# Kernel tuning notes

Hardware: AMD Instinct MI355X
Metric: run time of the kernel (lower is better)

The kernel has to match this reference:

```python
import jax, jax.numpy as jnp
import numpy as np
import math

B, S, H = 2, 2048, 4096
NH, HD = 32, 128            # num_heads, head_dim
Q_RANK, KV_RANK = 1536, 512 # low-rank dims
VD = 128                    # v_head_dim


def setup_inputs() -> dict:
    key = jax.random.key(0)
    ks = jax.random.split(key, 7)
    s = 0.02
    return {
        "hidden_states": jax.random.normal(ks[0], (B, S, H), dtype=jnp.float32),
        "w_qa":  jax.random.normal(ks[1], (H, Q_RANK), dtype=jnp.float32) * s,
        "w_qb":  jax.random.normal(ks[2], (Q_RANK, NH * HD), dtype=jnp.float32) * s,
        "w_kva": jax.random.normal(ks[3], (H, KV_RANK), dtype=jnp.float32) * s,
        "w_kb":  jax.random.normal(ks[4], (KV_RANK, NH * HD), dtype=jnp.float32) * s,
        "w_vb":  jax.random.normal(ks[5], (KV_RANK, NH * VD), dtype=jnp.float32) * s,
        "w_o":   jax.random.normal(ks[6], (NH * VD, H), dtype=jnp.float32) * s,
    }


def reference(hidden_states, w_qa, w_qb, w_kva, w_kb, w_vb, w_o):
    b, s, _ = hidden_states.shape
    # low-rank Q path
    q_c = hidden_states @ w_qa                       # [B,S,q_rank]
    q = (q_c @ w_qb).reshape(b, s, NH, HD)           # [B,S,NH,HD]
    # low-rank compressed KV (this is the cache tensor)
    compressed_kv = hidden_states @ w_kva            # [B,S,kv_rank]
    k = (compressed_kv @ w_kb).reshape(b, s, NH, HD)
    v = (compressed_kv @ w_vb).reshape(b, s, NH, VD)
    # causal SDPA, scale 1/sqrt(head_dim) (position_ids=None -> RoPE no-op)
    scale = 1.0 / math.sqrt(HD)
    scores = jnp.einsum('bqhd,bkhd->bhqk', q, k) * scale
    causal = jnp.tril(jnp.ones((s, s), dtype=bool))
    scores = jnp.where(causal, scores, jnp.finfo(scores.dtype).min)
    attn = jax.nn.softmax(scores, axis=-1)
    out = jnp.einsum('bhqk,bkhd->bqhd', attn, v).reshape(b, s, NH * VD)
    attn_output = out @ w_o                          # [B,S,H]
    return (attn_output, compressed_kv)
```

## Files before the change

### kernel.cpp

```cpp
#include <hip/hip_runtime.h>
#include <hip/hip_bf16.h>
#include <math.h>

#define BB 2
#define SS 2048
#define HH 4096
#define NHEADS 32
#define HDIM 128
#define VDIM 128
#define QRANK 1536
#define KVRANK 512
#define MROWS (BB * SS)

typedef unsigned short u16;
typedef unsigned int u32;
typedef short short8 __attribute__((ext_vector_type(8)));
typedef float floatx4 __attribute__((ext_vector_type(4)));

#if __has_builtin(__builtin_amdgcn_exp2f)
__device__ __forceinline__ float fast_exp2(float x) { return __builtin_amdgcn_exp2f(x); }
#else
__device__ __forceinline__ float fast_exp2(float x) { return exp2f(x); }
#endif

__device__ __forceinline__ u16 f2bf(float f) {
    u32 u = __float_as_uint(f);
    u += 0x7fffu + ((u >> 16) & 1u);
    return (u16)(u >> 16);
}

#define GLD16(gp, lp)                                                        \
    __builtin_amdgcn_global_load_lds(                                        \
        (const __attribute__((address_space(1))) void*)(gp),                 \
        (__attribute__((address_space(3))) void*)(lp), 16, 0, 0)

__global__ __launch_bounds__(256) void cvt_bf16(const float* __restrict__ in,
                                                u16* __restrict__ out, int n4) {
    int idx = blockIdx.x * 256 + threadIdx.x;
    int stride = gridDim.x * 256;
    for (int i = idx; i < n4; i += stride) {
        float4 f = ((const float4*)in)[i];
        u32 lo = (u32)f2bf(f.x) | ((u32)f2bf(f.y) << 16);
        u32 hi = (u32)f2bf(f.z) | ((u32)f2bf(f.w) << 16);
        ((uint2*)out)[i] = make_uint2(lo, hi);
    }
}

__global__ __launch_bounds__(256) void transpose_cvt(const float* __restrict__ in,
                                                     u16* __restrict__ out,
                                                     int R, int C) {
    __shared__ u16 T[64][65];
    const int c0 = blockIdx.x * 64, r0 = blockIdx.y * 64;
    const int tx = threadIdx.x & 63, ty = threadIdx.x >> 6;
#pragma unroll
    for (int p = 0; p < 16; ++p) {
        int rr = p * 4 + ty;
        T[rr][tx] = f2bf(in[(size_t)(r0 + rr) * C + c0 + tx]);
    }
    __syncthreads();
#pragma unroll
    for (int p = 0; p < 16; ++p) {
        int cc = p * 4 + ty;
        out[(size_t)(c0 + cc) * R + r0 + tx] = T[tx][cc];
    }
}

__global__ __launch_bounds__(256) void transpose_v(const u16* __restrict__ in, int ldin,
                                                   u16* __restrict__ out) {
    __shared__ u16 T[64][65];
    const int s0 = blockIdx.x * 64, d0 = blockIdx.y * 64;
    const int bh = blockIdx.z, b = bh >> 5, h = bh & 31;
    const int tx = threadIdx.x & 63, ty = threadIdx.x >> 6;
#pragma unroll
    for (int p = 0; p < 16; ++p) {
        int ss = p * 4 + ty;
        T[ss][tx] = in[(size_t)(b * SS + s0 + ss) * ldin + h * 128 + d0 + tx];
    }
    __syncthreads();
#pragma unroll
    for (int p = 0; p < 16; ++p) {
        int dd = p * 4 + ty;
        out[((size_t)bh * 128 + d0 + dd) * SS + s0 + tx] = T[tx][dd];
    }
}

template <int MODE>
__global__ __launch_bounds__(256) void gemm_bt(const u16* __restrict__ A, int lda,
                                               const u16* __restrict__ Bt, int ldb,
                                               float* __restrict__ Cf, int ldf,
                                               u16* __restrict__ Cb, int ldc,
                                               int M, int N, int K, int nsplit) {
    __shared__ __align__(16) u16 As[128 * 32];
    __shared__ __align__(16) u16 Bs[128 * 32];

    const int tid = threadIdx.x;
    const int bm0 = blockIdx.y * 128, bn0 = blockIdx.x * 128;
    const int w = tid >> 6, lane = tid & 63;
    const int lo = lane & 15, quad = lane >> 4;
    const int wm = (w & 1) * 64, wn = (w >> 1) * 64;

    floatx4 acc[4][4];
#pragma unroll
    for (int i = 0; i < 4; ++i)
#pragma unroll
        for (int j = 0; j < 4; ++j) acc[i][j] = (floatx4){0.f, 0.f, 0.f, 0.f};

    const int o0 = tid * 16, o1 = tid * 16 + 4096;
    const int ar0 = o0 >> 6, ak0 = (o0 & 63) >> 1;
    const int ar1 = o1 >> 6, ak1 = (o1 & 63) >> 1;
    const u16* Ab = A + (size_t)bm0 * lda;
    const u16* Bb = Bt + (size_t)bn0 * ldb;

    for (int k0 = 0; k0 < K; k0 += 32) {
        GLD16(Ab + (size_t)ar0 * lda + k0 + ak0, &As[o0 >> 1]);
        GLD16(Ab + (size_t)ar1 * lda + k0 + ak1, &As[o1 >> 1]);
        GLD16(Bb + (size_t)ar0 * ldb + k0 + ak0, &Bs[o0 >> 1]);
        GLD16(Bb + (size_t)ar1 * ldb + k0 + ak1, &Bs[o1 >> 1]);
        asm volatile("s_waitcnt vmcnt(0)" ::: "memory");
        __syncthreads();

        short8 af[4], bfr[4];
#pragma unroll
        for (int i = 0; i < 4; ++i)
            af[i] = *(const short8*)&As[(wm + i * 16 + lo) * 32 + quad * 8];
#pragma unroll
        for (int j = 0; j < 4; ++j)
            bfr[j] = *(const short8*)&Bs[(wn + j * 16 + lo) * 32 + quad * 8];
#pragma unroll
        for (int i = 0; i < 4; ++i)
#pragma unroll
            for (int j = 0; j < 4; ++j)
                acc[i][j] = __builtin_amdgcn_mfma_f32_16x16x32_bf16(af[i], bfr[j], acc[i][j], 0, 0, 0);
        __syncthreads();
    }

#pragma unroll
    for (int i = 0; i < 4; ++i) {
#pragma unroll
        for (int j = 0; j < 4; ++j) {
            const int row = bm0 + wm + i * 16 + quad * 4;
            const int col = bn0 + wn + j * 16 + lo;
#pragma unroll
            for (int r = 0; r < 4; ++r) {
                float v = acc[i][j][r];
                if (MODE == 0) Cf[(size_t)(row + r) * ldf + col] = v;
                if (MODE == 1) Cb[(size_t)(row + r) * ldc + col] = f2bf(v);
                if (MODE == 3) {
                    Cb[(size_t)(row + r) * ldc + col] = f2bf(v);
                    if (col >= nsplit) Cf[(size_t)(row + r) * ldf + (col - nsplit)] = v;
                }
            }
        }
    }
}

__global__ __launch_bounds__(256) void mla_attn_mfma(const u16* __restrict__ qm,
                                                     const u16* __restrict__ km, int ldk,
                                                     const u16* __restrict__ vt,
                                                     u16* __restrict__ ao) {
    __shared__ __align__(16) u16 Ks[64 * 128];
    __shared__ __align__(16) u16 Vt[(128 + 16) * 64];
    __shared__ __align__(16) u16 Ps[128 * 68];

    const int qt = 15 - blockIdx.y;
    const int bh = blockIdx.x;
    const int b = bh >> 5, h = bh & 31;
    const int tid = threadIdx.x;
    const int w = tid >> 6, lane = tid & 63;
    const int lo = lane & 15, quad = lane >> 4;
    const int q0 = qt * 128;

    const float SCALE_L2E = 0.08838834764831845f * 1.4426950408889634f;

    {
        u32* p = (u32*)&Vt[128 * 64];
        for (int i = tid; i < 512; i += 256) p[i] = 0x3F803F80u;
    }

    const u16* kbase = km + (size_t)(b * SS) * ldk + h * 128;
    const u16* vtbase = vt + (size_t)bh * 128 * SS;
    const int nkt = 2 * qt + 2;

    int ol_[4], kgo[4], vgo[4];
#pragma unroll
    for (int p = 0; p < 4; ++p) {
        int o = tid * 16 + p * 4096;
        int key = o >> 8, ch = (o & 255) >> 4;
        kgo[p] = key * ldk + ((ch ^ (key & 15)) << 3);
        int d = o >> 7, ch2 = (o & 127) >> 4;
        vgo[p] = d * SS + ((ch2 ^ (d & 7)) << 3);
        ol_[p] = o >> 1;
    }

#pragma unroll
    for (int p = 0; p < 4; ++p) GLD16(kbase + kgo[p], &Ks[ol_[p]]);
#pragma unroll
    for (int p = 0; p < 4; ++p) GLD16(vtbase + vgo[p], &Vt[ol_[p]]);

    short8 qf[2][4];
#pragma unroll
    for (int mf = 0; mf < 2; ++mf) {
        const u16* qrow = qm + (size_t)(b * SS + q0 + w * 32 + mf * 16 + lo) * HH + h * 128;
#pragma unroll
        for (int ks = 0; ks < 4; ++ks) qf[mf][ks] = *(const short8*)(qrow + ks * 32 + quad * 8);
    }

    floatx4 oacc[2][8], olv[2];
#pragma unroll
    for (int mf = 0; mf < 2; ++mf) {
        olv[mf] = (floatx4){0.f, 0.f, 0.f, 0.f};
#pragma unroll
        for (int n = 0; n < 8; ++n) oacc[mf][n] = (floatx4){0.f, 0.f, 0.f, 0.f};
    }

    __syncthreads();

    for (int kt = 0; kt < nkt; ++kt) {
        const bool need_mask = (kt >= nkt - 2);
        const bool notlast = (kt + 1 < nkt);

#pragma unroll
        for (int mf = 0; mf < 2; ++mf) {
            floatx4 s[4];
#pragma unroll
            for (int nf = 0; nf < 4; ++nf) s[nf] = (floatx4){0.f, 0.f, 0.f, 0.f};
            __builtin_amdgcn_s_setprio(1);
#pragma unroll
            for (int nf = 0; nf < 4; ++nf)
#pragma unroll
                for (int ks = 0; ks < 4; ++ks) {
                    short8 kf = *(const short8*)&Ks[(nf * 16 + lo) * 128 + (((ks * 4 + quad) ^ lo) << 3)];
                    s[nf] = __builtin_amdgcn_mfma_f32_16x16x32_bf16(qf[mf][ks], kf, s[nf], 0, 0, 0);
                }
            __builtin_amdgcn_s_setprio(0);
#pragma unroll
            for (int nf = 0; nf < 4; ++nf)
#pragma unroll
                for (int r = 0; r < 4; ++r) {
                    float p = fast_exp2(s[nf][r] * SCALE_L2E);
                    if (need_mask) {
                        int kgi = kt * 64 + nf * 16 + lo;
                        int qg = q0 + w * 32 + mf * 16 + quad * 4 + r;
                        p = (kgi <= qg) ? p : 0.f;
                    }
                    Ps[(w * 32 + mf * 16 + quad * 4 + r) * 68 + nf * 16 + lo] = f2bf(p);
                }
        }

        __syncthreads();

        if (notlast) {
            const u16* kn = kbase + (size_t)(kt + 1) * 64 * ldk;
#pragma unroll
            for (int p = 0; p < 4; ++p) GLD16(kn + kgo[p], &Ks[ol_[p]]);
        }

#pragma unroll
        for (int mf = 0; mf < 2; ++mf) {
            short8 pa[2];
#pragma unroll
            for (int ks2 = 0; ks2 < 2; ++ks2)
                pa[ks2] = *(const short8*)&Ps[(w * 32 + mf * 16 + lo) * 68 + ks2 * 32 + quad * 8];
            __builtin_amdgcn_s_setprio(1);
#pragma unroll
            for (int n = 0; n < 8; ++n)
#pragma unroll
                for (int ks2 = 0; ks2 < 2; ++ks2) {
                    short8 vf = *(const short8*)&Vt[(n * 16 + lo) * 64 + (((ks2 * 4 + quad) ^ (lo & 7)) << 3)];
                    oacc[mf][n] = __builtin_amdgcn_mfma_f32_16x16x32_bf16(pa[ks2], vf, oacc[mf][n], 0, 0, 0);
                }
#pragma unroll
            for (int ks2 = 0; ks2 < 2; ++ks2) {
                short8 vf = *(const short8*)&Vt[(128 + lo) * 64 + (((ks2 * 4 + quad) ^ (lo & 7)) << 3)];
                olv[mf] = __builtin_amdgcn_mfma_f32_16x16x32_bf16(pa[ks2], vf, olv[mf], 0, 0, 0);
            }
            __builtin_amdgcn_s_setprio(0);
        }

        __syncthreads();

        if (notlast) {
            const u16* vn = vtbase + (size_t)(kt + 1) * 64;
#pragma unroll
            for (int p = 0; p < 4; ++p) GLD16(vn + vgo[p], &Vt[ol_[p]]);
        }
    }

#pragma unroll
    for (int mf = 0; mf < 2; ++mf) {
        u16* obase = ao + (size_t)(b * SS + q0 + w * 32 + mf * 16 + quad * 4) * HH + h * 128;
#pragma unroll
        for (int r = 0; r < 4; ++r) {
            float inv = 1.f / olv[mf][r];
#pragma unroll
            for (int n = 0; n < 8; ++n)
                obase[(size_t)r * HH + n * 16 + lo] = f2bf(oacc[mf][n][r] * inv);
        }
    }
}

extern "C" void kernel_launch(void* const* d_in, const int* in_sizes, int n_in,
                              void* d_out, int out_size, void* d_ws, size_t ws_size,
                              hipStream_t stream) {
    const float* hs    = (const float*)d_in[0];
    const float* w_qa  = (const float*)d_in[1];
    const float* w_qb  = (const float*)d_in[2];
    const float* w_kva = (const float*)d_in[3];
    const float* w_kb  = (const float*)d_in[4];
    const float* w_vb  = (const float*)d_in[5];
    const float* w_o   = (const float*)d_in[6];

    float* out   = (float*)d_out;
    float* ckv_f = out + (size_t)MROWS * HH;

    u16* ws = (u16*)d_ws;
    u16* hs_bf    = ws;
    u16* vt       = ws;
    u16* q_bf     = ws + 16777216ull;
    u16* kv_bf    = ws + 33554432ull;
    u16* ao_bf    = ws + 67108864ull;
    u16* wqa_kvaT = ws + 83886080ull;
    u16* w_qbT    = ws + 92274688ull;
    u16* wkv_bT   = ws + 98566144ull;
    u16* w_oT     = ws + 102760448ull;
    u16* qc_ckv   = ws + 119537664ull;

    dim3 blk(256);

    cvt_bf16<<<2048, blk, 0, stream>>>(hs, hs_bf, (MROWS * HH) / 4);
    transpose_cvt<<<dim3(QRANK / 64, HH / 64), blk, 0, stream>>>(w_qa, wqa_kvaT, HH, QRANK);
    transpose_cvt<<<dim3(KVRANK / 64, HH / 64), blk, 0, stream>>>(w_kva, wqa_kvaT + 1536ull * 4096, HH, KVRANK);
    transpose_cvt<<<dim3(HH / 64, QRANK / 64), blk, 0, stream>>>(w_qb, w_qbT, QRANK, HH);
    transpose_cvt<<<dim3(HH / 64, KVRANK / 64), blk, 0, stream>>>(w_kb, wkv_bT, KVRANK, HH);
    transpose_cvt<<<dim3(HH / 64, KVRANK / 64), blk, 0, stream>>>(w_vb, wkv_bT + 4096ull * 512, KVRANK, HH);
    transpose_cvt<<<dim3(HH / 64, HH / 64), blk, 0, stream>>>(w_o, w_oT, HH, HH);

    gemm_bt<3><<<dim3(2048 / 128, MROWS / 128), blk, 0, stream>>>(
        hs_bf, HH, wqa_kvaT, HH, ckv_f, KVRANK, qc_ckv, 2048, MROWS, 2048, HH, QRANK);
    gemm_bt<1><<<dim3(HH / 128, MROWS / 128), blk, 0, stream>>>(
        qc_ckv, 2048, w_qbT, QRANK, nullptr, 0, q_bf, HH, MROWS, HH, QRANK, 0);
    gemm_bt<1><<<dim3(8192 / 128, MROWS / 128), blk, 0, stream>>>(
        qc_ckv + 1536, 2048, wkv_bT, KVRANK, nullptr, 0, kv_bf, 8192, MROWS, 8192, KVRANK, 0);
    transpose_v<<<dim3(SS / 64, VDIM / 64, BB * NHEADS), blk, 0, stream>>>(kv_bf + 4096, 8192, vt);
    mla_attn_mfma<<<dim3(BB * NHEADS, 16), blk, 0, stream>>>(q_bf, kv_bf, 8192, vt, ao_bf);
    gemm_bt<0><<<dim3(HH / 128, MROWS / 128), blk, 0, stream>>>(
        ao_bf, HH, w_oT, HH, out, HH, nullptr, 0, MROWS, HH, HH, 0);
}
```

Measured before the change: 811.2 us.

## Use 256x256 GEMM tiles with 4-stage async LDS pipeline and swizzle

Rewrites the bf16 GEMM to use 256x256 output tiles with 512 threads (8 waves, 128x64 per wave). Global-to-LDS loads now go through a 4-deep ring buffer with counted vmcnt waits, so loads overlap with MFMA work instead of waiting for all loads each k-step. An XOR swizzle on the LDS column chunk reduces bank conflicts, and s_setprio raises wave priority during the MFMA bursts. The trade-off is more LDS (128KB) and more registers per block, which lowers occupancy, and fewer blocks per GEMM (e.g. 128 for the first GEMM), which can leave CUs underused.

```diff
diff --git a/kernel.cpp b/kernel.cpp
--- a/kernel.cpp
+++ b/kernel.cpp
@@ -85,64 +85,97 @@
 }
 
 template <int MODE>
-__global__ __launch_bounds__(256) void gemm_bt(const u16* __restrict__ A, int lda,
+__global__ __launch_bounds__(512) void gemm_bt(const u16* __restrict__ A, int lda,
                                                const u16* __restrict__ Bt, int ldb,
                                                float* __restrict__ Cf, int ldf,
                                                u16* __restrict__ Cb, int ldc,
                                                int M, int N, int K, int nsplit) {
-    __shared__ __align__(16) u16 As[128 * 32];
-    __shared__ __align__(16) u16 Bs[128 * 32];
+    __shared__ __align__(16) u16 As[4][256 * 32];
+    __shared__ __align__(16) u16 Bs[4][256 * 32];
 
     const int tid = threadIdx.x;
-    const int bm0 = blockIdx.y * 128, bn0 = blockIdx.x * 128;
+    const int bm0 = blockIdx.y * 256, bn0 = blockIdx.x * 256;
     const int w = tid >> 6, lane = tid & 63;
     const int lo = lane & 15, quad = lane >> 4;
-    const int wm = (w & 1) * 64, wn = (w >> 1) * 64;
-
-    floatx4 acc[4][4];
-#pragma unroll
-    for (int i = 0; i < 4; ++i)
-#pragma unroll
-        for (int j = 0; j < 4; ++j) acc[i][j] = (floatx4){0.f, 0.f, 0.f, 0.f};
-
-    const int o0 = tid * 16, o1 = tid * 16 + 4096;
-    const int ar0 = o0 >> 6, ak0 = (o0 & 63) >> 1;
-    const int ar1 = o1 >> 6, ak1 = (o1 & 63) >> 1;
+    const int wm = (w >> 2) * 128, wn = (w & 3) * 64;
+
+    floatx4 acc[8][4];
+#pragma unroll
+    for (int m = 0; m < 8; ++m)
+#pragma unroll
+        for (int n = 0; n < 4; ++n) acc[m][n] = (floatx4){0.f, 0.f, 0.f, 0.f};
+
+    int row_[2], gco[2], ldso[2];
+#pragma unroll
+    for (int p = 0; p < 2; ++p) {
+        int o = tid * 16 + p * 8192;
+        row_[p] = o >> 6;
+        int c = (o & 63) >> 4;
+        gco[p] = ((c ^ ((row_[p] >> 1) & 3)) << 3);
+        ldso[p] = o >> 1;
+    }
+
     const u16* Ab = A + (size_t)bm0 * lda;
     const u16* Bb = Bt + (size_t)bn0 * ldb;
-
-    for (int k0 = 0; k0 < K; k0 += 32) {
-        GLD16(Ab + (size_t)ar0 * lda + k0 + ak0, &As[o0 >> 1]);
-        GLD16(Ab + (size_t)ar1 * lda + k0 + ak1, &As[o1 >> 1]);
-        GLD16(Bb + (size_t)ar0 * ldb + k0 + ak0, &Bs[o0 >> 1]);
-        GLD16(Bb + (size_t)ar1 * ldb + k0 + ak1, &Bs[o1 >> 1]);
-        asm volatile("s_waitcnt vmcnt(0)" ::: "memory");
-        __syncthreads();
-
-        short8 af[4], bfr[4];
-#pragma unroll
-        for (int i = 0; i < 4; ++i)
-            af[i] = *(const short8*)&As[(wm + i * 16 + lo) * 32 + quad * 8];
-#pragma unroll
-        for (int j = 0; j < 4; ++j)
-            bfr[j] = *(const short8*)&Bs[(wn + j * 16 + lo) * 32 + quad * 8];
-#pragma unroll
-        for (int i = 0; i < 4; ++i)
-#pragma unroll
-            for (int j = 0; j < 4; ++j)
-                acc[i][j] = __builtin_amdgcn_mfma_f32_16x16x32_bf16(af[i], bfr[j], acc[i][j], 0, 0, 0);
-        __syncthreads();
-    }
-
-#pragma unroll
-    for (int i = 0; i < 4; ++i) {
-#pragma unroll
-        for (int j = 0; j < 4; ++j) {
-            const int row = bm0 + wm + i * 16 + quad * 4;
-            const int col = bn0 + wn + j * 16 + lo;
+    const int NT = K >> 5;
+
+    auto STAGE = [&](int t) {
+        const int s = t & 3;
+        const int k0 = t << 5;
+#pragma unroll
+        for (int p = 0; p < 2; ++p)
+            GLD16(Ab + (size_t)row_[p] * lda + k0 + gco[p], &As[s][ldso[p]]);
+#pragma unroll
+        for (int p = 0; p < 2; ++p)
+            GLD16(Bb + (size_t)row_[p] * ldb + k0 + gco[p], &Bs[s][ldso[p]]);
+    };
+
+    STAGE(0);
+    if (NT > 1) STAGE(1);
+    if (NT > 2) STAGE(2);
+
+    for (int kt = 0; kt < NT; ++kt) {
+        __builtin_amdgcn_s_barrier();
+        if (kt + 3 < NT) STAGE(kt + 3);
+        __builtin_amdgcn_sched_barrier(0);
+        if (kt < NT - 3)       asm volatile("s_waitcnt vmcnt(12)" ::: "memory");
+        else if (kt == NT - 3) asm volatile("s_waitcnt vmcnt(8)" ::: "memory");
+        else if (kt == NT - 2) asm volatile("s_waitcnt vmcnt(4)" ::: "memory");
+        else                   asm volatile("s_waitcnt vmcnt(0)" ::: "memory");
+        __builtin_amdgcn_sched_barrier(0);
+        __builtin_amdgcn_s_barrier();
+        __builtin_amdgcn_sched_barrier(0);
+
+        const int s = kt & 3;
+        short8 af[8], bfr[4];
+#pragma unroll
+        for (int m = 0; m < 8; ++m) {
+            const int r = wm + m * 16 + lo;
+            af[m] = *(const short8*)&As[s][r * 32 + ((quad ^ ((r >> 1) & 3)) << 3)];
+        }
+#pragma unroll
+        for (int n = 0; n < 4; ++n) {
+            const int r = wn + n * 16 + lo;
+            bfr[n] = *(const short8*)&Bs[s][r * 32 + ((quad ^ ((r >> 1) & 3)) << 3)];
+        }
+        __builtin_amdgcn_s_setprio(1);
+#pragma unroll
+        for (int m = 0; m < 8; ++m)
+#pragma unroll
+            for (int n = 0; n < 4; ++n)
+                acc[m][n] = __builtin_amdgcn_mfma_f32_16x16x32_bf16(af[m], bfr[n], acc[m][n], 0, 0, 0);
+        __builtin_amdgcn_s_setprio(0);
+    }
+
+#pragma unroll
+    for (int m = 0; m < 8; ++m) {
+#pragma unroll
+        for (int n = 0; n < 4; ++n) {
+            const int row = bm0 + wm + m * 16 + quad * 4;
+            const int col = bn0 + wn + n * 16 + lo;
 #pragma unroll
             for (int r = 0; r < 4; ++r) {
-                float v = acc[i][j][r];
+                float v = acc[m][n][r];
                 if (MODE == 0) Cf[(size_t)(row + r) * ldf + col] = v;
                 if (MODE == 1) Cb[(size_t)(row + r) * ldc + col] = f2bf(v);
                 if (MODE == 3) {
@@ -326,6 +359,7 @@
     u16* qc_ckv   = ws + 119537664ull;
 
     dim3 blk(256);
+    dim3 blkg(512);
 
     cvt_bf16<<<2048, blk, 0, stream>>>(hs, hs_bf, (MROWS * HH) / 4);
     transpose_cvt<<<dim3(QRANK / 64, HH / 64), blk, 0, stream>>>(w_qa, wqa_kvaT, HH, QRANK);
@@ -335,14 +369,14 @@
     transpose_cvt<<<dim3(HH / 64, KVRANK / 64), blk, 0, stream>>>(w_vb, wkv_bT + 4096ull * 512, KVRANK, HH);
     transpose_cvt<<<dim3(HH / 64, HH / 64), blk, 0, stream>>>(w_o, w_oT, HH, HH);
 
-    gemm_bt<3><<<dim3(2048 / 128, MROWS / 128), blk, 0, stream>>>(
+    gemm_bt<3><<<dim3(2048 / 256, MROWS / 256), blkg, 0, stream>>>(
         hs_bf, HH, wqa_kvaT, HH, ckv_f, KVRANK, qc_ckv, 2048, MROWS, 2048, HH, QRANK);
-    gemm_bt<1><<<dim3(HH / 128, MROWS / 128), blk, 0, stream>>>(
+    gemm_bt<1><<<dim3(HH / 256, MROWS / 256), blkg, 0, stream>>>(
         qc_ckv, 2048, w_qbT, QRANK, nullptr, 0, q_bf, HH, MROWS, HH, QRANK, 0);
-    gemm_bt<1><<<dim3(8192 / 128, MROWS / 128), blk, 0, stream>>>(
+    gemm_bt<1><<<dim3(8192 / 256, MROWS / 256), blkg, 0, stream>>>(
         qc_ckv + 1536, 2048, wkv_bT, KVRANK, nullptr, 0, kv_bf, 8192, MROWS, 8192, KVRANK, 0);
     transpose_v<<<dim3(SS / 64, VDIM / 64, BB * NHEADS), blk, 0, stream>>>(kv_bf + 4096, 8192, vt);
     mla_attn_mfma<<<dim3(BB * NHEADS, 16), blk, 0, stream>>>(q_bf, kv_bf, 8192, vt, ao_bf);
-    gemm_bt<0><<<dim3(HH / 128, MROWS / 128), blk, 0, stream>>>(
+    gemm_bt<0><<<dim3(HH / 256, MROWS / 256), blkg, 0, stream>>>(
         ao_bf, HH, w_oT, HH, out, HH, nullptr, 0, MROWS, HH, HH, 0);
 }
```

Measured after the change: 799.2 us. No clear change (-1.5%).
